# Optimization experiments

Hardware: AMD Instinct MI355X
Metric: run time of the kernel (lower is better)

The kernel has to match this reference:

```python
import jax, jax.numpy as jnp
import numpy as np

KH = KW = 3
K = KH * KW
STRIDE = 1
PAD = 1
DIL = 1
DG = 1  # deformable groups


def conv2d(x, w, b):
    out = jax.lax.conv_general_dilated(
        x, w, window_strides=(STRIDE, STRIDE),
        padding=[(PAD, PAD), (PAD, PAD)], rhs_dilation=(DIL, DIL),
        dimension_numbers=('NCHW', 'OIHW', 'NCHW'))
    return out + b[None, :, None, None]


def deform_conv2d(x, offset, mask, w, b):
    """DCNv2: bilinear sample at predicted offsets, modulate by mask, GEMM with w."""
    B, Cin, H, W = x.shape
    Ho, Wo = offset.shape[2], offset.shape[3]
    cpg = Cin // DG
    # torchvision layout: channel 2*(g*K+k) = dy, 2*(g*K+k)+1 = dx
    off = offset.reshape(B, DG, K, 2, Ho, Wo)
    off_y, off_x = off[:, :, :, 0], off[:, :, :, 1]  # [B,DG,K,Ho,Wo]
    m = mask.reshape(B, DG, K, Ho, Wo)
    ky = jnp.repeat(jnp.arange(KH), KW) * DIL          # [K] kernel row offsets
    kx = jnp.tile(jnp.arange(KW), KH) * DIL            # [K] kernel col offsets
    hh = jnp.arange(Ho) * STRIDE - PAD
    ww = jnp.arange(Wo) * STRIDE - PAD
    py = off_y + ky[None, None, :, None, None] + hh[None, None, None, :, None]
    px = off_x + kx[None, None, :, None, None] + ww[None, None, None, None, :]
    y0 = jnp.floor(py); x0 = jnp.floor(px)
    wy = py - y0; wx = px - x0
    x_g = x.reshape(B, DG, cpg, H * W)

    def gather(yc, xc):  # zero-padded bilinear corner fetch
        valid = ((yc >= 0) & (yc < H) & (xc >= 0) & (xc < W)).astype(x.dtype)
        yi = jnp.clip(yc, 0, H - 1).astype(jnp.int32)
        xi = jnp.clip(xc, 0, W - 1).astype(jnp.int32)
        idx = (yi * W + xi).reshape(B, DG, 1, K * Ho * Wo)
        v = jnp.take_along_axis(x_g, jnp.broadcast_to(idx, (B, DG, cpg, K * Ho * Wo)), axis=3)
        return v.reshape(B, DG, cpg, K, Ho, Wo) * valid[:, :, None]

    v00 = gather(y0, x0)
    v01 = gather(y0, x0 + 1)
    v10 = gather(y0 + 1, x0)
    v11 = gather(y0 + 1, x0 + 1)
    wy_b = wy[:, :, None]; wx_b = wx[:, :, None]  # broadcast over cpg
    sampled = (v00 * (1 - wy_b) * (1 - wx_b) + v01 * (1 - wy_b) * wx_b
               + v10 * wy_b * (1 - wx_b) + v11 * wy_b * wx_b)
    sampled = (sampled * m[:, :, None]).reshape(B, Cin, K, Ho, Wo)
    Cout = w.shape[0]
    out = jnp.einsum('bckhw,ock->bohw', sampled, w.reshape(Cout, Cin, K))
    return out + b[None, :, None, None]


def setup_inputs() -> dict:
    key = jax.random.key(0)
    k1, k2, k3, k4 = jax.random.split(key, 4)
    B, Cin, Cout, H, W = 8, 128, 128, 64, 64
    omc = DG * 3 * K  # 2*K offsets + K mask channels = 27
    x = jax.random.normal(k1, (B, Cin, H, W), dtype=jnp.float32)
    # small offset-conv weights -> modest predicted offsets (mimics near-zero init)
    w_off = jax.random.normal(k2, (omc, Cin, KH, KW), dtype=jnp.float32) * 0.01
    b_off = jnp.zeros((omc,), dtype=jnp.float32)
    w_def = jax.random.normal(k3, (Cout, Cin, KH, KW), dtype=jnp.float32) * (1.0 / np.sqrt(Cin * K))
    b_def = jax.random.normal(k4, (Cout,), dtype=jnp.float32) * 0.01
    return {"x": x, "w_off": w_off, "b_off": b_off, "w_def": w_def, "b_def": b_def}


def reference(x, w_off, b_off, w_def, b_def):
    out = conv2d(x, w_off, b_off)
    oc = DG * 2 * K
    offset = out[:, :oc]
    mask = jax.nn.sigmoid(out[:, oc:])
    return deform_conv2d(x, offset, mask, w_def, b_def)
```

## Files before the change

kernel.cpp:

```cpp
#include <hip/hip_runtime.h>
#include <math.h>

typedef _Float16 f16;
typedef __attribute__((ext_vector_type(2))) _Float16 f16x2;
typedef __attribute__((ext_vector_type(4))) _Float16 f16x4;
typedef __attribute__((ext_vector_type(8))) _Float16 f16x8;
typedef __attribute__((ext_vector_type(4))) float f32x4;

#define NBATCH 8
#define WSA_ELE 36864
#define WSB_ELE 147456
#define PREP_BLOCKS 720
#define OFF_WSB  73728
#define OFF_XT   368640

__device__ __forceinline__ void gload_lds16(const f16* gsrc, f16* ldst) {
  __builtin_amdgcn_global_load_lds(
      (const __attribute__((address_space(1))) unsigned int*)gsrc,
      (__attribute__((address_space(3))) unsigned int*)ldst, 16, 0, 0);
}

__global__ __launch_bounds__(256) void prep_transpose_kernel(const float* __restrict__ w_off,
                                                             const float* __restrict__ w_def,
                                                             f16* __restrict__ wsA,
                                                             f16* __restrict__ wsB,
                                                             const float* __restrict__ x,
                                                             f16* __restrict__ xt) {
  __shared__ __align__(16) f16 s_t[128 * 68];
  const int t = threadIdx.x;
  if (blockIdx.x < PREP_BLOCKS) {
    int i = blockIdx.x * 256 + t;
    if (i < WSA_ELE) {
      int j = i & 7, lane = (i >> 3) & 63, fm = i >> 9;
      int ch = fm >> 1, mt = fm & 1;
      int row = mt * 16 + (lane & 15);
      int kidx = ch * 32 + (lane >> 4) * 8 + j;
      int k = kidx >> 7, cc = kidx & 127;
      float v = (row < 27) ? w_off[row * 1152 + cc * 9 + k] : 0.0f;
      wsA[i] = (f16)v;
    } else {
      int e = i - WSA_ELE;
      int j = e & 7, lane = (e >> 3) & 63, fm = e >> 9;
      int ch = fm >> 3, mt = fm & 7;
      int row = mt * 16 + (lane & 15);
      int kidx = ch * 32 + (lane >> 4) * 8 + j;
      int k = kidx >> 7, cc = kidx & 127;
      wsB[e] = (f16)w_def[row * 1152 + cc * 9 + k];
    }
    return;
  }
  const int bid = blockIdx.x - PREP_BLOCKS;
  const int b = bid >> 6;
  const int pos0 = (bid & 63) << 6;
  const float* xb = x + ((size_t)b << 19);
  #pragma unroll
  for (int it = 0; it < 8; ++it) {
    int i = it * 256 + t;
    int c = i >> 4, p4 = (i & 15) << 2;
    float4 v = *(const float4*)&xb[c * 4096 + pos0 + p4];
    f16x4 h = {(f16)v.x, (f16)v.y, (f16)v.z, (f16)v.w};
    *(f16x4*)&s_t[c * 68 + p4] = h;
  }
  __syncthreads();
  f16* xtb = xt + ((size_t)b << 19);
  #pragma unroll
  for (int it = 0; it < 8; ++it) {
    int i = it * 256 + t;
    int p = i >> 5, c4 = (i & 31) << 2;
    f16x4 h = {s_t[(c4    ) * 68 + p],
               s_t[(c4 + 1) * 68 + p],
               s_t[(c4 + 2) * 68 + p],
               s_t[(c4 + 3) * 68 + p]};
    *(f16x4*)&xtb[(size_t)(pos0 + p) * 128 + c4] = h;
  }
}

__global__ __launch_bounds__(256, 2) void fused_dcn_kernel(const f16* __restrict__ xt,
                                                           const f16* __restrict__ wsA,
                                                           const f16* __restrict__ wsB,
                                                           const float* __restrict__ b_off,
                                                           const float* __restrict__ b_def,
                                                           float* __restrict__ out) {
  __shared__ float  s_off[27 * 65];
  __shared__ uint4  s_ofs[576];
  __shared__ float4 s_wt[576];
  __shared__ __align__(16) f16 s_a[3 * 8192];
  const int t = threadIdx.x;
  const int b = blockIdx.x & 7, ho = blockIdx.x >> 3;
  const int lane = t & 63, wid = t >> 6;
  const int q = lane >> 4, li = lane & 15;
  const int px = (wid << 4) + li;
  const char* xtb = (const char*)xt + ((size_t)b << 20);

  #pragma unroll
  for (int j = 0; j < 4; ++j) {
    gload_lds16(wsB +        (wid * 4 + j) * 512 + lane * 8, s_a +        (wid * 4 + j) * 512);
    gload_lds16(wsB + 8192 + (wid * 4 + j) * 512 + lane * 8, s_a + 8192 + (wid * 4 + j) * 512);
  }

  {
    f32x4 acc0 = {0.f, 0.f, 0.f, 0.f}, acc1 = {0.f, 0.f, 0.f, 0.f};
    #pragma unroll
    for (int k = 0; k < 9; ++k) {
      const int ky = k / 3, kx = k - ky * 3;
      const int y = ho + ky - 1;
      const int xx = px + kx - 1;
      const bool valid = ((unsigned)y < 64u) && ((unsigned)xx < 64u);
      const int pos = min(max(y, 0), 63) * 64 + min(max(xx, 0), 63);
      const int voff = pos * 256 + q * 16;
      #pragma unroll
      for (int c4 = 0; c4 < 4; ++c4) {
        union { uint4 u; f16x8 v; } bu;
        bu.u = *(const uint4*)(xtb + voff + c4 * 64);
        if (!valid) { bu.u.x = 0u; bu.u.y = 0u; bu.u.z = 0u; bu.u.w = 0u; }
        const int ch = k * 4 + c4;
        f16x8 a0 = *(const f16x8*)&wsA[(ch * 2    ) * 512 + lane * 8];
        f16x8 a1 = *(const f16x8*)&wsA[(ch * 2 + 1) * 512 + lane * 8];
        acc0 = __builtin_amdgcn_mfma_f32_16x16x32_f16(a0, bu.v, acc0, 0, 0, 0);
        acc1 = __builtin_amdgcn_mfma_f32_16x16x32_f16(a1, bu.v, acc1, 0, 0, 0);
      }
    }
    #pragma unroll
    for (int mt = 0; mt < 2; ++mt) {
      f32x4 a = mt ? acc1 : acc0;
      #pragma unroll
      for (int r = 0; r < 4; ++r) {
        int oc = mt * 16 + q * 4 + r;
        if (oc < 27) {
          float v = a[r] + b_off[oc];
          if (oc >= 18) v = 1.0f / (1.0f + __expf(-v));
          s_off[oc * 65 + px] = v;
        }
      }
    }
  }
  __syncthreads();

  for (int f = t; f < 576; f += 256) {
    int k = f >> 6, p = f & 63;
    int ky = k / 3, kx = k - ky * 3;
    float oy = s_off[(2 * k    ) * 65 + p];
    float ox = s_off[(2 * k + 1) * 65 + p];
    float m  = s_off[(18 + k   ) * 65 + p];
    float py  = oy + (float)(ho + ky - 1);
    float pxf = ox + (float)(p + kx - 1);
    float y0f = floorf(py), x0f = floorf(pxf);
    float wy = py - y0f, wx = pxf - x0f;
    int y0 = (int)y0f, x0 = (int)x0f;
    int y1 = y0 + 1, x1 = x0 + 1;
    bool y0v = (unsigned)y0 < 64u, y1v = (unsigned)y1 < 64u;
    bool x0v = (unsigned)x0 < 64u, x1v = (unsigned)x1 < 64u;
    int y0c = min(max(y0, 0), 63), y1c = min(max(y1, 0), 63);
    int x0c = min(max(x0, 0), 63), x1c = min(max(x1, 0), 63);
    uint4 o4;
    o4.x = (unsigned)((y0c * 64 + x0c) * 256);
    o4.y = (unsigned)((y0c * 64 + x1c) * 256);
    o4.z = (unsigned)((y1c * 64 + x0c) * 256);
    o4.w = (unsigned)((y1c * 64 + x1c) * 256);
    float4 w4;
    w4.x = (y0v && x0v) ? (1.f - wy) * (1.f - wx) * m : 0.f;
    w4.y = (y0v && x1v) ? (1.f - wy) * wx         * m : 0.f;
    w4.z = (y1v && x0v) ? wy         * (1.f - wx) * m : 0.f;
    w4.w = (y1v && x1v) ? wy         * wx         * m : 0.f;
    s_ofs[f] = o4;
    s_wt[f]  = w4;
  }
  __syncthreads();

  f32x4 acc[8];
  #pragma unroll
  for (int mt = 0; mt < 8; ++mt) acc[mt] = (f32x4){0.f, 0.f, 0.f, 0.f};

  typedef union { uint4 u; f16x2 h[4]; } AU;
  AU Gc[8], Gn[8];

  {
    const uint4 o4 = s_ofs[px];
    #pragma unroll
    for (int cc = 0; cc < 2; ++cc) {
      const unsigned add = q * 16 + cc * 64;
      Gc[cc * 4 + 0].u = *(const uint4*)(xtb + o4.x + add);
      Gc[cc * 4 + 1].u = *(const uint4*)(xtb + o4.y + add);
      Gc[cc * 4 + 2].u = *(const uint4*)(xtb + o4.z + add);
      Gc[cc * 4 + 3].u = *(const uint4*)(xtb + o4.w + add);
    }
  }

  #pragma unroll 2
  for (int h = 0; h < 18; ++h) {
    if (h < 17) { asm volatile("s_waitcnt vmcnt(12)" ::: "memory"); }
    else        { asm volatile("s_waitcnt vmcnt(8)"  ::: "memory"); }
    __builtin_amdgcn_s_barrier();

    if (h < 17) {
      const int hn = h + 1;
      const int kn = hn >> 1;
      const uint4 o4 = s_ofs[kn * 64 + px];
      #pragma unroll
      for (int cc = 0; cc < 2; ++cc) {
        const unsigned add = q * 16 + (((hn << 1) + cc) & 3) * 64;
        Gn[cc * 4 + 0].u = *(const uint4*)(xtb + o4.x + add);
        Gn[cc * 4 + 1].u = *(const uint4*)(xtb + o4.y + add);
        Gn[cc * 4 + 2].u = *(const uint4*)(xtb + o4.z + add);
        Gn[cc * 4 + 3].u = *(const uint4*)(xtb + o4.w + add);
      }
    }
    if (h < 16) {
      const int hs = h + 2;
      const f16* src = wsB + hs * 8192 + (wid * 4) * 512;
      f16* dst = s_a + (hs % 3) * 8192 + (wid * 4) * 512;
      #pragma unroll
      for (int j = 0; j < 4; ++j)
        gload_lds16(src + j * 512 + lane * 8, dst + j * 512);
    }
    asm volatile("" ::: "memory");

    const f16* abuf = s_a + (h % 3) * 8192;
    #pragma unroll
    for (int cc = 0; cc < 2; ++cc) {
      const int ch = (h << 1) + cc;
      const float4 w4 = s_wt[(ch >> 2) * 64 + px];
      const f16 h0 = (f16)w4.x, h1 = (f16)w4.y, h2 = (f16)w4.z, h3 = (f16)w4.w;
      const f16x2 wp0 = {h0, h0}, wp1 = {h1, h1}, wp2 = {h2, h2}, wp3 = {h3, h3};
      union { f16x2 h[4]; f16x8 v; } bf;
      #pragma unroll
      for (int i = 0; i < 4; ++i) {
        f16x2 s = Gc[cc * 4 + 0].h[i] * wp0;
        s = s + Gc[cc * 4 + 1].h[i] * wp1;
        s = s + Gc[cc * 4 + 2].h[i] * wp2;
        s = s + Gc[cc * 4 + 3].h[i] * wp3;
        bf.h[i] = s;
      }
      const f16* ab = abuf + cc * 4096;
      #pragma unroll
      for (int mt = 0; mt < 8; ++mt) {
        f16x8 a = *(const f16x8*)&ab[(mt * 64 + lane) * 8];
        acc[mt] = __builtin_amdgcn_mfma_f32_16x16x32_f16(a, bf.v, acc[mt], 0, 0, 0);
      }
    }
    #pragma unroll
    for (int i = 0; i < 8; ++i) Gc[i] = Gn[i];
  }

  float* o = out + (size_t)b * 128 * 4096 + ho * 64 + px;
  #pragma unroll
  for (int mt = 0; mt < 8; ++mt) {
    #pragma unroll
    for (int r = 0; r < 4; ++r) {
      int oc = mt * 16 + q * 4 + r;
      o[oc * 4096] = acc[mt][r] + b_def[oc];
    }
  }
}

extern "C" void kernel_launch(void* const* d_in, const int* in_sizes, int n_in,
                              void* d_out, int out_size, void* d_ws, size_t ws_size,
                              hipStream_t stream) {
  const float* x     = (const float*)d_in[0];
  const float* w_off = (const float*)d_in[1];
  const float* b_off = (const float*)d_in[2];
  const float* w_def = (const float*)d_in[3];
  const float* b_def = (const float*)d_in[4];
  float* out = (float*)d_out;

  f16* wsA = (f16*)d_ws;
  f16* wsB = (f16*)((char*)d_ws + OFF_WSB);
  f16* xt  = (f16*)((char*)d_ws + OFF_XT);

  prep_transpose_kernel<<<dim3(PREP_BLOCKS + NBATCH * 64), dim3(256), 0, stream>>>(
      w_off, w_def, wsA, wsB, x, xt);
  fused_dcn_kernel<<<dim3(NBATCH * 64), dim3(256), 0, stream>>>(
      xt, wsA, wsB, b_off, b_def, out);
}
```

Measured before the change: 130.8 us.

## Process two output rows per 512-thread block, sharing staged weight tiles

Each block now handles two output rows with 8 waves instead of one row with 4 waves. The staged deformable-weight tiles in LDS are shared across both rows, so each wave issues half as many global-to-LDS loads per stage. Bilinear weights are also stored as f16x4 in shared memory instead of float4, which cuts LDS use and removes the per-iteration conversions. The grid halves to 256 blocks with one block per CU allowed, which may reduce occupancy and latency hiding on a 256-CU part.

```diff
diff --git a/kernel.cpp b/kernel.cpp
--- a/kernel.cpp
+++ b/kernel.cpp
@@ -75,35 +75,39 @@
   }
 }
 
-__global__ __launch_bounds__(256, 2) void fused_dcn_kernel(const f16* __restrict__ xt,
+__global__ __launch_bounds__(512, 1) void fused_dcn_kernel(const f16* __restrict__ xt,
                                                            const f16* __restrict__ wsA,
                                                            const f16* __restrict__ wsB,
                                                            const float* __restrict__ b_off,
                                                            const float* __restrict__ b_def,
                                                            float* __restrict__ out) {
-  __shared__ float  s_off[27 * 65];
-  __shared__ uint4  s_ofs[576];
-  __shared__ float4 s_wt[576];
+  __shared__ float  s_off[2 * 27 * 65];
+  __shared__ uint4  s_ofs[2 * 576];
+  __shared__ f16x4  s_wth[2 * 576];
   __shared__ __align__(16) f16 s_a[3 * 8192];
   const int t = threadIdx.x;
-  const int b = blockIdx.x & 7, ho = blockIdx.x >> 3;
+  const int b = blockIdx.x & 7;
+  const int hp = blockIdx.x >> 3;
   const int lane = t & 63, wid = t >> 6;
+  const int row = wid >> 2;
+  const int rowy = hp * 2 + row;
   const int q = lane >> 4, li = lane & 15;
-  const int px = (wid << 4) + li;
+  const int px = ((wid & 3) << 4) + li;
   const char* xtb = (const char*)xt + ((size_t)b << 20);
 
   #pragma unroll
-  for (int j = 0; j < 4; ++j) {
-    gload_lds16(wsB +        (wid * 4 + j) * 512 + lane * 8, s_a +        (wid * 4 + j) * 512);
-    gload_lds16(wsB + 8192 + (wid * 4 + j) * 512 + lane * 8, s_a + 8192 + (wid * 4 + j) * 512);
+  for (int j = 0; j < 2; ++j) {
+    gload_lds16(wsB +        (wid * 2 + j) * 512 + lane * 8, s_a +        (wid * 2 + j) * 512);
+    gload_lds16(wsB + 8192 + (wid * 2 + j) * 512 + lane * 8, s_a + 8192 + (wid * 2 + j) * 512);
   }
 
   {
+    float* so = s_off + row * (27 * 65);
     f32x4 acc0 = {0.f, 0.f, 0.f, 0.f}, acc1 = {0.f, 0.f, 0.f, 0.f};
     #pragma unroll
     for (int k = 0; k < 9; ++k) {
       const int ky = k / 3, kx = k - ky * 3;
-      const int y = ho + ky - 1;
+      const int y = rowy + ky - 1;
       const int xx = px + kx - 1;
       const bool valid = ((unsigned)y < 64u) && ((unsigned)xx < 64u);
       const int pos = min(max(y, 0), 63) * 64 + min(max(xx, 0), 63);
@@ -129,20 +133,22 @@
         if (oc < 27) {
           float v = a[r] + b_off[oc];
           if (oc >= 18) v = 1.0f / (1.0f + __expf(-v));
-          s_off[oc * 65 + px] = v;
+          so[oc * 65 + px] = v;
         }
       }
     }
   }
   __syncthreads();
 
-  for (int f = t; f < 576; f += 256) {
-    int k = f >> 6, p = f & 63;
+  for (int f = t; f < 1152; f += 512) {
+    int r = f / 576, e = f - r * 576;
+    int k = e >> 6, p = e & 63;
     int ky = k / 3, kx = k - ky * 3;
-    float oy = s_off[(2 * k    ) * 65 + p];
-    float ox = s_off[(2 * k + 1) * 65 + p];
-    float m  = s_off[(18 + k   ) * 65 + p];
-    float py  = oy + (float)(ho + ky - 1);
+    const float* so = s_off + r * (27 * 65);
+    float oy = so[(2 * k    ) * 65 + p];
+    float ox = so[(2 * k + 1) * 65 + p];
+    float m  = so[(18 + k   ) * 65 + p];
+    float py  = oy + (float)(hp * 2 + r + ky - 1);
     float pxf = ox + (float)(p + kx - 1);
     float y0f = floorf(py), x0f = floorf(pxf);
     float wy = py - y0f, wx = pxf - x0f;
@@ -157,25 +163,28 @@
     o4.y = (unsigned)((y0c * 64 + x1c) * 256);
     o4.z = (unsigned)((y1c * 64 + x0c) * 256);
     o4.w = (unsigned)((y1c * 64 + x1c) * 256);
-    float4 w4;
-    w4.x = (y0v && x0v) ? (1.f - wy) * (1.f - wx) * m : 0.f;
-    w4.y = (y0v && x1v) ? (1.f - wy) * wx         * m : 0.f;
-    w4.z = (y1v && x0v) ? wy         * (1.f - wx) * m : 0.f;
-    w4.w = (y1v && x1v) ? wy         * wx         * m : 0.f;
+    float w0 = (y0v && x0v) ? (1.f - wy) * (1.f - wx) * m : 0.f;
+    float w1 = (y0v && x1v) ? (1.f - wy) * wx         * m : 0.f;
+    float w2 = (y1v && x0v) ? wy         * (1.f - wx) * m : 0.f;
+    float w3 = (y1v && x1v) ? wy         * wx         * m : 0.f;
     s_ofs[f] = o4;
-    s_wt[f]  = w4;
+    f16x4 wp = {(f16)w0, (f16)w1, (f16)w2, (f16)w3};
+    s_wth[f] = wp;
   }
   __syncthreads();
 
   f32x4 acc[8];
   #pragma unroll
   for (int mt = 0; mt < 8; ++mt) acc[mt] = (f32x4){0.f, 0.f, 0.f, 0.f};
+
+  const uint4* ofs = s_ofs + row * 576;
+  const f16x4* wtb = s_wth + row * 576;
 
   typedef union { uint4 u; f16x2 h[4]; } AU;
   AU Gc[8], Gn[8];
 
   {
-    const uint4 o4 = s_ofs[px];
+    const uint4 o4 = ofs[px];
     #pragma unroll
     for (int cc = 0; cc < 2; ++cc) {
       const unsigned add = q * 16 + cc * 64;
@@ -188,14 +197,13 @@
 
   #pragma unroll 2
   for (int h = 0; h < 18; ++h) {
-    if (h < 17) { asm volatile("s_waitcnt vmcnt(12)" ::: "memory"); }
+    if (h < 17) { asm volatile("s_waitcnt vmcnt(10)" ::: "memory"); }
     else        { asm volatile("s_waitcnt vmcnt(8)"  ::: "memory"); }
     __builtin_amdgcn_s_barrier();
 
     if (h < 17) {
       const int hn = h + 1;
-      const int kn = hn >> 1;
-      const uint4 o4 = s_ofs[kn * 64 + px];
+      const uint4 o4 = ofs[(hn >> 1) * 64 + px];
       #pragma unroll
       for (int cc = 0; cc < 2; ++cc) {
         const unsigned add = q * 16 + (((hn << 1) + cc) & 3) * 64;
@@ -207,11 +215,10 @@
     }
     if (h < 16) {
       const int hs = h + 2;
-      const f16* src = wsB + hs * 8192 + (wid * 4) * 512;
-      f16* dst = s_a + (hs % 3) * 8192 + (wid * 4) * 512;
-      #pragma unroll
-      for (int j = 0; j < 4; ++j)
-        gload_lds16(src + j * 512 + lane * 8, dst + j * 512);
+      const f16* src = wsB + hs * 8192 + (wid * 2) * 512;
+      f16* dst = s_a + (hs % 3) * 8192 + (wid * 2) * 512;
+      gload_lds16(src +       lane * 8, dst);
+      gload_lds16(src + 512 + lane * 8, dst + 512);
     }
     asm volatile("" ::: "memory");
 
@@ -219,9 +226,9 @@
     #pragma unroll
     for (int cc = 0; cc < 2; ++cc) {
       const int ch = (h << 1) + cc;
-      const float4 w4 = s_wt[(ch >> 2) * 64 + px];
-      const f16 h0 = (f16)w4.x, h1 = (f16)w4.y, h2 = (f16)w4.z, h3 = (f16)w4.w;
-      const f16x2 wp0 = {h0, h0}, wp1 = {h1, h1}, wp2 = {h2, h2}, wp3 = {h3, h3};
+      const f16x4 wp = wtb[(ch >> 2) * 64 + px];
+      const f16x2 wp0 = {wp.x, wp.x}, wp1 = {wp.y, wp.y};
+      const f16x2 wp2 = {wp.z, wp.z}, wp3 = {wp.w, wp.w};
       union { f16x2 h[4]; f16x8 v; } bf;
       #pragma unroll
       for (int i = 0; i < 4; ++i) {
@@ -242,7 +249,7 @@
     for (int i = 0; i < 8; ++i) Gc[i] = Gn[i];
   }
 
-  float* o = out + (size_t)b * 128 * 4096 + ho * 64 + px;
+  float* o = out + (size_t)b * 128 * 4096 + rowy * 64 + px;
   #pragma unroll
   for (int mt = 0; mt < 8; ++mt) {
     #pragma unroll
@@ -269,6 +276,6 @@
 
   prep_transpose_kernel<<<dim3(PREP_BLOCKS + NBATCH * 64), dim3(256), 0, stream>>>(
       w_off, w_def, wsA, wsB, x, xt);
-  fused_dcn_kernel<<<dim3(NBATCH * 64), dim3(256), 0, stream>>>(
+  fused_dcn_kernel<<<dim3(NBATCH * 32), dim3(512), 0, stream>>>(
       xt, wsA, wsB, b_off, b_def, out);
 }
```

After: 132.1 us. No clear change (+1.0%).
